# Kernel optimization log

Measured on AMD Instinct MI355X. Metric: run time of the kernel, lower is better.

## Reference

```python
import jax, jax.numpy as jnp
import numpy as np

N_ENT, N_CON, DIM, R, NB = 30000, 29309, 128, 12, 8
B, LC, S, E_DB, E_CON = 256, 50, 32, 300000, 200000


def setup_inputs() -> dict:
    key = jax.random.key(0)
    ks = jax.random.split(key, 32)
    f = lambda k, sh: (jax.random.normal(k, sh, jnp.float32) * 0.02)
    concept_emb = f(ks[0], (N_CON, DIM)).at[0].set(0.0)  # padding_idx=0 row zeroed
    inp = {
        'concept_mask': jax.random.randint(ks[1], (B, LC), 0, N_CON, jnp.int32),
        'seed_pad': jax.random.randint(ks[2], (B, S), 0, N_ENT, jnp.int32),
        'seed_lens': jax.random.randint(ks[3], (B,), 0, S + 1, jnp.int32),
        'db_edge_index': jax.random.randint(ks[4], (2, E_DB), 0, N_ENT, jnp.int32),
        'db_edge_type': jax.random.randint(ks[5], (E_DB,), 0, R, jnp.int32),
        'con_edge_index': jax.random.randint(ks[6], (2, E_CON), 0, N_CON, jnp.int32),
        'db_vec': jax.random.uniform(ks[7], (B, N_ENT), jnp.float32),
        'labels': jax.random.randint(ks[8], (B,), 0, N_ENT, jnp.int64),
        'rec': jax.random.uniform(ks[9], (B,), jnp.float32),
        'concept_emb': concept_emb,
        'basis': f(ks[10], (NB, N_ENT, DIM)),
        'comp': f(ks[11], (R, NB)),
        'rgcn_root': f(ks[12], (N_ENT, DIM)),
        'rgcn_bias': jnp.zeros((DIM,), jnp.float32),
        'gcn_w': f(ks[13], (DIM, DIM)),
        'gcn_b': jnp.zeros((DIM,), jnp.float32),
        'attn_a': f(ks[14], (DIM, DIM)),
        'attn_b': f(ks[15], (DIM, 1)),
        'attn_a_db': f(ks[16], (DIM, DIM)),
        'attn_b_db': f(ks[17], (DIM, 1)),
        'user_norm_w': f(ks[18], (DIM, 2 * DIM)),
        'user_norm_b': jnp.zeros((DIM,), jnp.float32),
        'gate_norm_w': f(ks[19], (1, DIM)),
        'gate_norm_b': jnp.zeros((1,), jnp.float32),
        'info_con_w': f(ks[20], (DIM, DIM)),
        'info_con_b': jnp.zeros((DIM,), jnp.float32),
        'info_out_db_b': jnp.zeros((N_ENT,), jnp.float32),
        'output_en_b': jnp.zeros((N_ENT,), jnp.float32),
    }
    return inp


def _forward(concept_mask, seed_pad, seed_lens, db_edge_index, db_edge_type,
             con_edge_index, db_vec, labels, rec, concept_emb, basis, comp,
             rgcn_root, rgcn_bias, gcn_w, gcn_b, attn_a, attn_b, attn_a_db,
             attn_b_db, user_norm_w, user_norm_b, gate_norm_w, gate_norm_b,
             info_con_w, info_con_b, info_out_db_b, output_en_b):
    NEG = jnp.float32(-1e30)
    # ---- RGCN over DBpedia graph (x=None -> per-edge row W[rel][src]) ----
    w = jnp.einsum('rb,bnd->rnd', comp, basis)            # [R, N_ent, D]
    src, dst = db_edge_index[0], db_edge_index[1]
    msg = w[db_edge_type, src]                            # [E, D]
    agg = jax.ops.segment_sum(msg, dst, num_segments=N_ENT)
    cnt = jax.ops.segment_sum(jnp.ones_like(dst, jnp.float32), dst, num_segments=N_ENT)
    db_feats = agg / jnp.maximum(cnt, 1.0)[:, None] + rgcn_root + rgcn_bias  # mean aggr + root + bias
    # ---- GCN over concept graph (symmetric norm, self-loops) ----
    xw = concept_emb @ gcn_w
    loops = jnp.arange(N_CON, dtype=con_edge_index.dtype)
    cs = jnp.concatenate([con_edge_index[0], loops])
    cd = jnp.concatenate([con_edge_index[1], loops])
    deg = jax.ops.segment_sum(jnp.ones_like(cd, jnp.float32), cd, num_segments=N_CON)
    dinv = jnp.where(deg > 0, jax.lax.rsqrt(jnp.maximum(deg, 1e-12)), 0.0)
    norm = dinv[cs] * dinv[cd]
    con_feats = jax.ops.segment_sum(norm[:, None] * xw[cs], cd, num_segments=N_CON) + gcn_b
    # ---- per-sample seed-set self-attention over db features ----
    h = db_feats[seed_pad]                                # [B, S, D]
    e = jnp.tanh(h @ attn_a_db) @ attn_b_db               # [B, S, 1]
    valid = jnp.arange(S)[None, :] < seed_lens[:, None]   # [B, S]
    a = jax.nn.softmax(jnp.where(valid[..., None], e, NEG), axis=1)
    db_user = jnp.einsum('bso,bsd->bd', a, h)             # weighted sum (o=1)
    has_seed = (seed_lens > 0)
    db_user = jnp.where(has_seed[:, None], db_user, 0.0)  # empty seed set -> zeros
    db_con_mask = has_seed.astype(jnp.float32)
    # ---- batch self-attention over gathered concept features ----
    hc = con_feats[concept_mask]                          # [B, LC, D]
    ec = jnp.tanh(hc @ attn_a) @ attn_b                   # [B, LC, 1]
    cvalid = (concept_mask != 0)
    ac = jax.nn.softmax(jnp.where(cvalid[..., None], ec, NEG), axis=1)
    con_user = jnp.einsum('blo,bld->bd', ac, hc)
    # ---- gated fusion ----
    u = jnp.concatenate([con_user, db_user], axis=-1) @ user_norm_w.T + user_norm_b
    gate = jax.nn.sigmoid(u @ gate_norm_w.T + gate_norm_b)  # [B, 1]
    user_emb = gate * db_user + (1.0 - gate) * con_user
    entity_scores = user_emb @ db_feats.T + output_en_b   # [B, N_ent]
    # ---- infomax MSE loss ----
    con_e = con_user @ info_con_w.T + info_con_b
    db_scores = con_e @ db_feats.T + info_out_db_b
    info_db_loss = jnp.mean(jnp.sum((db_scores - db_vec) ** 2, axis=-1) * db_con_mask)
    # ---- rec CE loss ----
    logp = jax.nn.log_softmax(entity_scores, axis=-1)
    ce = -jnp.take_along_axis(logp, labels[:, None].astype(jnp.int32), axis=1)[:, 0]
    rec_loss = jnp.sum(ce * rec)
    loss = rec_loss + 0.025 * info_db_loss                # pretrain=False path
    return loss, entity_scores, rec_loss


def reference(concept_mask, seed_pad, seed_lens, db_edge_index, db_edge_type,
              con_edge_index, db_vec, labels, rec, concept_emb, basis, comp,
              rgcn_root, rgcn_bias, gcn_w, gcn_b, attn_a, attn_b, attn_a_db,
              attn_b_db, user_norm_w, user_norm_b, gate_norm_w, gate_norm_b,
              info_con_w, info_con_b, info_out_db_b, output_en_b):
    return _forward(concept_mask, seed_pad, seed_lens, db_edge_index, db_edge_type,
                    con_edge_index, db_vec, labels, rec, concept_emb, basis, comp,
                    rgcn_root, rgcn_bias, gcn_w, gcn_b, attn_a, attn_b, attn_a_db,
                    attn_b_db, user_norm_w, user_norm_b, gate_norm_w, gate_norm_b,
                    info_con_w, info_con_b, info_out_db_b, output_en_b)
```

## Files before the change

### kernel.cpp

```cpp
#include <hip/hip_runtime.h>

#define N_ENT  30000
#define N_CON  29309
#define DIM    128
#define NBASIS 8
#define NREL   12
#define BATCH  256
#define LCON   50
#define SSEED  32
#define EDB    300000
#define ECON   200000
#define NTILE  938

#define NE4      ((N_CON * DIM) / 4)
#define NB_HIST  ((EDB + ECON + 255) / 256)
#define NB_CONV  ((NE4 + 3 * (DIM * DIM / 4) + 255) / 256)
#define NB_WCOMP ((N_ENT * 32) / 256)
#define NB_GXW   ((N_CON + 31) / 32)
#define NB_RG    ((N_ENT + 3) / 4)
#define NB_GG    ((N_CON + 3) / 4)
#define NB_EDB   ((N_ENT + 31) / 32)
#define NB_ECON  ((N_CON + 31) / 32)

typedef __attribute__((ext_vector_type(8)))  short bfrag8;
typedef __attribute__((ext_vector_type(16))) float facc16;

__device__ __forceinline__ unsigned short f2bf(float f) {
    unsigned int u = __float_as_uint(f);
    u += 0x7FFFu + ((u >> 16) & 1u);
    return (unsigned short)(u >> 16);
}
__device__ __forceinline__ float bf2f(unsigned int h) {
    return __uint_as_float(h << 16);
}

__global__ __launch_bounds__(256) void prep_kernel(const int* __restrict__ db_dst,
                                                   const int* __restrict__ con_dst,
                                                   const float* __restrict__ emb,
                                                   const float* __restrict__ W,
                                                   const float* __restrict__ A_db,
                                                   const float* __restrict__ A_c,
                                                   int* __restrict__ cnt_e, int* __restrict__ cnt_c,
                                                   int* __restrict__ ord_db, int* __restrict__ ord_con,
                                                   unsigned short* __restrict__ emb_h,
                                                   unsigned short* __restrict__ Wt_h,
                                                   unsigned short* __restrict__ At_db_h,
                                                   unsigned short* __restrict__ At_c_h) {
    int t = threadIdx.x, bb = blockIdx.x;
    if (bb < NB_HIST) {
        int e = bb * 256 + t;
        if (e < EDB) {
            ord_db[e] = atomicAdd(cnt_e + db_dst[e], 1);
        } else if (e < EDB + ECON) {
            int ee = e - EDB;
            ord_con[ee] = atomicAdd(cnt_c + con_dst[ee], 1);
        }
    } else {
        int i = (bb - NB_HIST) * 256 + t;
        if (i < NE4) {
            float4 v = ((const float4*)emb)[i];
            unsigned int p0 = (unsigned int)f2bf(v.x) | ((unsigned int)f2bf(v.y) << 16);
            unsigned int p1 = (unsigned int)f2bf(v.z) | ((unsigned int)f2bf(v.w) << 16);
            *(uint2*)(emb_h + (size_t)i * 4) = make_uint2(p0, p1);
        } else {
            int j = i - NE4;
            if (j < 3 * (DIM * DIM) / 4) {
                int sel = j >> 12;
                int jj = j & 4095;
                const float* S = (sel == 0) ? W : ((sel == 1) ? A_db : A_c);
                unsigned short* Dst = (sel == 0) ? Wt_h : ((sel == 1) ? At_db_h : At_c_h);
                int o = jj * 4;
                int n = o >> 7, k0 = o & 127;
                unsigned int p0 = (unsigned int)f2bf(S[(k0 + 0) * DIM + n]) |
                                  ((unsigned int)f2bf(S[(k0 + 1) * DIM + n]) << 16);
                unsigned int p1 = (unsigned int)f2bf(S[(k0 + 2) * DIM + n]) |
                                  ((unsigned int)f2bf(S[(k0 + 3) * DIM + n]) << 16);
                *(uint2*)(Dst + n * DIM + k0) = make_uint2(p0, p1);
            }
        }
    }
}

__device__ void scan_block(const int* __restrict__ cnt, int n, int* __restrict__ rowptr) {
    __shared__ int part[1024];
    int t = threadIdx.x;
    int per = (n + 1023) / 1024;
    int s0 = t * per;
    int sum = 0;
    for (int i = 0; i < per; ++i) {
        int idx = s0 + i;
        if (idx < n) sum += cnt[idx];
    }
    part[t] = sum;
    __syncthreads();
    for (int off = 1; off < 1024; off <<= 1) {
        int v = (t >= off) ? part[t - off] : 0;
        __syncthreads();
        part[t] += v;
        __syncthreads();
    }
    int run = part[t] - sum;
    for (int i = 0; i < per; ++i) {
        int idx = s0 + i;
        if (idx < n) {
            rowptr[idx] = run;
            run += cnt[idx];
        }
    }
    if (t == 1023) rowptr[n] = part[1023];
}

__global__ __launch_bounds__(1024) void scan2_kernel(const int* __restrict__ cnt_e,
                                                     const int* __restrict__ cnt_c,
                                                     int* __restrict__ rowptr_e,
                                                     int* __restrict__ rowptr_c,
                                                     float* __restrict__ dinv) {
    if (blockIdx.x == 0) {
        scan_block(cnt_e, N_ENT, rowptr_e);
    } else {
        scan_block(cnt_c, N_CON, rowptr_c);
        for (int i = threadIdx.x; i < N_CON; i += 1024)
            dinv[i] = rsqrtf((float)(cnt_c[i] + 1));
    }
}

__global__ __launch_bounds__(256) void mid_kernel(const int* __restrict__ db_eidx,
                                                  const int* __restrict__ db_etype,
                                                  const int* __restrict__ con_eidx,
                                                  const int* __restrict__ ord_db,
                                                  const int* __restrict__ ord_con,
                                                  const int* __restrict__ rowptr_e,
                                                  const int* __restrict__ rowptr_c,
                                                  int* __restrict__ elist_e,
                                                  int* __restrict__ elist_c,
                                                  const float* __restrict__ basis,
                                                  const float* __restrict__ comp,
                                                  unsigned short* __restrict__ w_h,
                                                  const unsigned short* __restrict__ emb_h,
                                                  const unsigned short* __restrict__ Wt_h,
                                                  unsigned short* __restrict__ xw_h,
                                                  int use_w) {
    __shared__ float sc[NREL * NBASIS];
    int t = threadIdx.x, bb = blockIdx.x;
    if (bb < NB_HIST) {
        int e = bb * 256 + t;
        if (e < EDB) {
            int dst = db_eidx[EDB + e];
            elist_e[rowptr_e[dst] + ord_db[e]] = db_eidx[e] | (db_etype[e] << 18);
        } else if (e < EDB + ECON) {
            int ee = e - EDB;
            int dst = con_eidx[ECON + ee];
            elist_c[rowptr_c[dst] + ord_con[ee]] = con_eidx[ee];
        }
        return;
    }
    if (bb < NB_HIST + NB_WCOMP) {
        if (!use_w) return;
        if (t < NREL * NBASIS) sc[t] = comp[t];
        __syncthreads();
        int i = (bb - NB_HIST) * 256 + t;
        int n = i >> 5, d4 = i & 31;
        float4 bv[NBASIS];
#pragma unroll
        for (int b = 0; b < NBASIS; ++b)
            bv[b] = ((const float4*)(basis + ((size_t)b * N_ENT + n) * DIM))[d4];
#pragma unroll
        for (int r = 0; r < NREL; ++r) {
            float4 acc = make_float4(0.f, 0.f, 0.f, 0.f);
#pragma unroll
            for (int b = 0; b < NBASIS; ++b) {
                float c = sc[r * NBASIS + b];
                acc.x += c * bv[b].x; acc.y += c * bv[b].y;
                acc.z += c * bv[b].z; acc.w += c * bv[b].w;
            }
            unsigned int p0 = (unsigned int)f2bf(acc.x) | ((unsigned int)f2bf(acc.y) << 16);
            unsigned int p1 = (unsigned int)f2bf(acc.z) | ((unsigned int)f2bf(acc.w) << 16);
            *(uint2*)(w_h + ((size_t)r * N_ENT + n) * DIM + d4 * 4) = make_uint2(p0, p1);
        }
        return;
    }
    {
        int gb = bb - NB_HIST - NB_WCOMP;
        int wave = t >> 6, lane = t & 63;
        int m0 = gb * 32;
        int n0 = wave * 32;
        int am = lane & 31, ak = (lane >> 5) * 8;
        int mrow = m0 + am;
        bool mv = mrow < N_CON;
        const unsigned short* Ar = emb_h + (size_t)mrow * DIM + ak;
        const unsigned short* Br = Wt_h + (size_t)(n0 + am) * DIM + ak;
        facc16 acc;
#pragma unroll
        for (int r = 0; r < 16; ++r) acc[r] = 0.f;
#pragma unroll
        for (int s = 0; s < 8; ++s) {
            bfrag8 a;
#pragma unroll
            for (int j = 0; j < 8; ++j) a[j] = 0;
            if (mv) a = *(const bfrag8*)(Ar + s * 16);
            bfrag8 b = *(const bfrag8*)(Br + s * 16);
            acc = __builtin_amdgcn_mfma_f32_32x32x16_bf16(a, b, acc, 0, 0, 0);
        }
        int col = lane & 31;
        int g4 = (lane >> 5) * 4;
#pragma unroll
        for (int r = 0; r < 16; ++r) {
            int m = m0 + (r & 3) + ((r >> 2) << 3) + g4;
            if (m < N_CON) xw_h[(size_t)m * DIM + n0 + col] = f2bf(acc[r]);
        }
    }
}

__global__ __launch_bounds__(256) void gathers_kernel(const int* __restrict__ rowptr_e,
                                                      const int* __restrict__ elist_e,
                                                      const unsigned short* __restrict__ w_h,
                                                      const float* __restrict__ root,
                                                      const float* __restrict__ bias,
                                                      unsigned short* __restrict__ dbf_h,
                                                      const int* __restrict__ rowptr_c,
                                                      const int* __restrict__ elist_c,
                                                      const float* __restrict__ dinv,
                                                      const unsigned short* __restrict__ xw_h,
                                                      const float* __restrict__ gcn_b,
                                                      unsigned short* __restrict__ conf_h) {
    int bb = blockIdx.x;
    int lane = threadIdx.x & 63;
    if (bb < NB_RG) {
        int wid = bb * 4 + (threadIdx.x >> 6);
        if (wid >= N_ENT) return;
        int beg = rowptr_e[wid], end = rowptr_e[wid + 1];
        float a0 = 0.f, a1 = 0.f;
        int p = beg;
        for (; p + 1 < end; p += 2) {
            int v0 = elist_e[p], v1 = elist_e[p + 1];
            unsigned int k0 = *(const unsigned int*)(w_h + ((size_t)(v0 >> 18) * N_ENT + (v0 & 0x3FFFF)) * DIM + lane * 2);
            unsigned int k1 = *(const unsigned int*)(w_h + ((size_t)(v1 >> 18) * N_ENT + (v1 & 0x3FFFF)) * DIM + lane * 2);
            a0 += bf2f(k0 & 0xFFFF) + bf2f(k1 & 0xFFFF);
            a1 += bf2f(k0 >> 16)    + bf2f(k1 >> 16);
        }
        if (p < end) {
            int v = elist_e[p];
            unsigned int k = *(const unsigned int*)(w_h + ((size_t)(v >> 18) * N_ENT + (v & 0x3FFFF)) * DIM + lane * 2);
            a0 += bf2f(k & 0xFFFF);
            a1 += bf2f(k >> 16);
        }
        float inv = 1.f / fmaxf((float)(end - beg), 1.f);
        size_t base = (size_t)wid * DIM + lane * 2;
        float f0 = a0 * inv + root[base]     + bias[lane * 2];
        float f1 = a1 * inv + root[base + 1] + bias[lane * 2 + 1];
        *(unsigned int*)(dbf_h + base) = (unsigned int)f2bf(f0) | ((unsigned int)f2bf(f1) << 16);
    } else {
        int wid = (bb - NB_RG) * 4 + (threadIdx.x >> 6);
        if (wid >= N_CON) return;
        int beg = rowptr_c[wid], end = rowptr_c[wid + 1];
        float a0 = 0.f, a1 = 0.f;
        int p = beg;
        for (; p + 1 < end; p += 2) {
            int s0 = elist_c[p], s1 = elist_c[p + 1];
            float n0 = dinv[s0], n1 = dinv[s1];
            unsigned int k0 = *(const unsigned int*)(xw_h + (size_t)s0 * DIM + lane * 2);
            unsigned int k1 = *(const unsigned int*)(xw_h + (size_t)s1 * DIM + lane * 2);
            a0 += n0 * bf2f(k0 & 0xFFFF) + n1 * bf2f(k1 & 0xFFFF);
            a1 += n0 * bf2f(k0 >> 16)    + n1 * bf2f(k1 >> 16);
        }
        if (p < end) {
            int s = elist_c[p];
            float nm = dinv[s];
            unsigned int k = *(const unsigned int*)(xw_h + (size_t)s * DIM + lane * 2);
            a0 += nm * bf2f(k & 0xFFFF);
            a1 += nm * bf2f(k >> 16);
        }
        float dv = dinv[wid];
        unsigned int ks = *(const unsigned int*)(xw_h + (size_t)wid * DIM + lane * 2);
        size_t base = (size_t)wid * DIM + lane * 2;
        float f0 = dv * a0 + dv * dv * bf2f(ks & 0xFFFF) + gcn_b[lane * 2];
        float f1 = dv * a1 + dv * dv * bf2f(ks >> 16)    + gcn_b[lane * 2 + 1];
        *(unsigned int*)(conf_h + base) = (unsigned int)f2bf(f0) | ((unsigned int)f2bf(f1) << 16);
    }
}

__global__ __launch_bounds__(256) void rgcn_gather_basis(const int* __restrict__ rowptr,
                                                         const int* __restrict__ elist,
                                                         const float* __restrict__ basis,
                                                         const float* __restrict__ comp,
                                                         const float* __restrict__ root,
                                                         const float* __restrict__ bias,
                                                         unsigned short* __restrict__ dbf_h) {
    int wid  = blockIdx.x * 4 + (threadIdx.x >> 6);
    int lane = threadIdx.x & 63;
    if (wid >= N_ENT) return;
    int beg = rowptr[wid], end = rowptr[wid + 1];
    float a0 = 0.f, a1 = 0.f;
    for (int p = beg; p < end; ++p) {
        int v = elist[p];
        int src = v & 0x3FFFF, ty = v >> 18;
        const float* c = comp + ty * NBASIS;
#pragma unroll
        for (int b = 0; b < NBASIS; ++b) {
            const float* bp = basis + ((size_t)b * N_ENT + src) * DIM;
            a0 += c[b] * bp[lane * 2];
            a1 += c[b] * bp[lane * 2 + 1];
        }
    }
    float inv = 1.f / fmaxf((float)(end - beg), 1.f);
    size_t base = (size_t)wid * DIM + lane * 2;
    float f0 = a0 * inv + root[base]     + bias[lane * 2];
    float f1 = a1 * inv + root[base + 1] + bias[lane * 2 + 1];
    *(unsigned int*)(dbf_h + base) = (unsigned int)f2bf(f0) | ((unsigned int)f2bf(f1) << 16);
}

__global__ __launch_bounds__(256) void escore_kernel(const unsigned short* __restrict__ dbf_h,
                                                     const unsigned short* __restrict__ conf_h,
                                                     const unsigned short* __restrict__ At_db_h,
                                                     const float* __restrict__ v_db,
                                                     const unsigned short* __restrict__ At_c_h,
                                                     const float* __restrict__ v_c,
                                                     float* __restrict__ e_db,
                                                     float* __restrict__ e_con) {
    __shared__ float part[4][32];
    int t = threadIdx.x, bb = blockIdx.x;
    int wave = t >> 6, lane = t & 63;
    const unsigned short* feats;
    const unsigned short* At;
    const float* v;
    float* eo;
    int m0, nrow;
    if (bb < NB_EDB) {
        feats = dbf_h;  At = At_db_h; v = v_db; eo = e_db;  m0 = bb * 32;             nrow = N_ENT;
    } else {
        feats = conf_h; At = At_c_h;  v = v_c;  eo = e_con; m0 = (bb - NB_EDB) * 32;  nrow = N_CON;
    }
    int n0 = wave * 32;
    int am = lane & 31, ak = (lane >> 5) * 8;
    int mrow = m0 + am;
    bool mv = mrow < nrow;
    const unsigned short* Ar = feats + (size_t)mrow * DIM + ak;
    const unsigned short* Br = At + (size_t)(n0 + am) * DIM + ak;
    facc16 acc;
#pragma unroll
    for (int r = 0; r < 16; ++r) acc[r] = 0.f;
#pragma unroll
    for (int s = 0; s < 8; ++s) {
        bfrag8 a;
#pragma unroll
        for (int j = 0; j < 8; ++j) a[j] = 0;
        if (mv) a = *(const bfrag8*)(Ar + s * 16);
        bfrag8 b = *(const bfrag8*)(Br + s * 16);
        acc = __builtin_amdgcn_mfma_f32_32x32x16_bf16(a, b, acc, 0, 0, 0);
    }
    int col = lane & 31, g = lane >> 5;
    float vn = v[n0 + col];
#pragma unroll
    for (int r = 0; r < 16; ++r) {
        float x = tanhf(acc[r]) * vn;
#pragma unroll
        for (int off = 16; off >= 1; off >>= 1) x += __shfl_xor(x, off, 32);
        if (col == 0) {
            int row = (r & 3) + ((r >> 2) << 3) + (g << 2);
            part[wave][row] = x;
        }
    }
    __syncthreads();
    if (t < 32) {
        int m = m0 + t;
        if (m < nrow)
            eo[m] = part[0][t] + part[1][t] + part[2][t] + part[3][t];
    }
}

__global__ __launch_bounds__(256) void attn_fusion_kernel(const unsigned short* __restrict__ dbf_h,
                                                          const unsigned short* __restrict__ conf_h,
                                                          const float* __restrict__ e_db,
                                                          const float* __restrict__ e_con,
                                                          const int* __restrict__ seed_pad,
                                                          const int* __restrict__ seed_lens,
                                                          const int* __restrict__ concept_mask,
                                                          const float* __restrict__ Wu, const float* __restrict__ bu,
                                                          const float* __restrict__ gw, const float* __restrict__ gb,
                                                          const float* __restrict__ Wi, const float* __restrict__ bi,
                                                          unsigned short* __restrict__ uemb_h,
                                                          unsigned short* __restrict__ cone_h,
                                                          float* __restrict__ maskv) {
    __shared__ int srow[SSEED];
    __shared__ int crow[LCON];
    __shared__ float a_db[SSEED], a_con[LCON];
    __shared__ float du[DIM], cu[DIM], red[DIM];
    int b = blockIdx.x, t = threadIdx.x;
    int wave = t >> 6, lane = t & 63;
    int len = seed_lens[b];
    if (wave == 0) {
        float e = -1e30f;
        if (lane < SSEED) {
            int rv = seed_pad[b * SSEED + lane];
            srow[lane] = rv;
            if (lane < len) e = e_db[rv];
        }
        float m = e;
#pragma unroll
        for (int off = 16; off >= 1; off >>= 1) m = fmaxf(m, __shfl_xor(m, off, 32));
        float p = (lane < SSEED) ? __expf(e - m) : 0.f;
        float s = p;
#pragma unroll
        for (int off = 16; off >= 1; off >>= 1) s += __shfl_xor(s, off, 32);
        if (lane < SSEED) a_db[lane] = p / s;
    } else if (wave == 1) {
        float e = -1e30f;
        if (lane < LCON) {
            int rv = concept_mask[b * LCON + lane];
            crow[lane] = rv;
            if (rv != 0) e = e_con[rv];
        }
        float m = e;
#pragma unroll
        for (int off = 32; off >= 1; off >>= 1) m = fmaxf(m, __shfl_xor(m, off, 64));
        float p = (lane < LCON) ? __expf(e - m) : 0.f;
        float s = p;
#pragma unroll
        for (int off = 32; off >= 1; off >>= 1) s += __shfl_xor(s, off, 64);
        if (lane < LCON) a_con[lane] = p / s;
    }
    __syncthreads();
    if (t < DIM) {
        float acc = 0.f;
#pragma unroll
        for (int s = 0; s < SSEED; ++s)
            acc += a_db[s] * bf2f((unsigned int)dbf_h[(size_t)srow[s] * DIM + t]);
        du[t] = (len > 0) ? acc : 0.f;
    } else {
        int d = t - DIM;
        float acc = 0.f;
#pragma unroll
        for (int s = 0; s < LCON; ++s)
            acc += a_con[s] * bf2f((unsigned int)conf_h[(size_t)crow[s] * DIM + d]);
        cu[d] = acc;
    }
    __syncthreads();
    if (t < DIM) {
        float u = bu[t];
        const float* wr = Wu + t * 2 * DIM;
        for (int k = 0; k < DIM; ++k) u += cu[k] * wr[k];
        for (int k = 0; k < DIM; ++k) u += du[k] * wr[DIM + k];
        red[t] = u * gw[t];
    }
    __syncthreads();
    for (int s2 = 64; s2 > 0; s2 >>= 1) {
        if (t < s2) red[t] += red[t + s2];
        __syncthreads();
    }
    if (t < DIM) {
        float gate = 1.f / (1.f + __expf(-(red[0] + gb[0])));
        uemb_h[b * DIM + t] = f2bf(gate * du[t] + (1.f - gate) * cu[t]);
        float ce = bi[t];
        const float* wi = Wi + t * DIM;
        for (int k = 0; k < DIM; ++k) ce += cu[k] * wi[k];
        cone_h[b * DIM + t] = f2bf(ce);
    }
    if (t == 0) maskv[b] = (len > 0) ? 1.f : 0.f;
}

__global__ __launch_bounds__(256) void score_mfma(const unsigned short* __restrict__ dbf_h,
                                                  const unsigned short* __restrict__ uemb_h,
                                                  const unsigned short* __restrict__ cone_h,
                                                  const float* __restrict__ en_b,
                                                  const float* __restrict__ info_b,
                                                  const float* __restrict__ db_vec,
                                                  float* __restrict__ escore,
                                                  float* __restrict__ partM,
                                                  float* __restrict__ partS,
                                                  float* __restrict__ partQ) {
    int wave = threadIdx.x >> 6, lane = threadIdx.x & 63;
    int nt = blockIdx.x * 4 + wave;
    if (nt >= NTILE) return;
    int b0 = blockIdx.y * 32;
    int n0 = nt * 32;
    int am = lane & 31, ak = (lane >> 5) * 8;
    int nb = n0 + am;
    bool bvalid = nb < N_ENT;
    const unsigned short* Au = uemb_h + (size_t)(b0 + am) * DIM + ak;
    const unsigned short* Ac = cone_h + (size_t)(b0 + am) * DIM + ak;
    const unsigned short* Bp = dbf_h + (size_t)nb * DIM + ak;
    facc16 accE, accD;
#pragma unroll
    for (int r = 0; r < 16; ++r) { accE[r] = 0.f; accD[r] = 0.f; }
#pragma unroll
    for (int s = 0; s < 8; ++s) {
        bfrag8 au = *(const bfrag8*)(Au + s * 16);
        bfrag8 ac = *(const bfrag8*)(Ac + s * 16);
        bfrag8 bb;
#pragma unroll
        for (int j = 0; j < 8; ++j) bb[j] = 0;
        if (bvalid) bb = *(const bfrag8*)(Bp + s * 16);
        accE = __builtin_amdgcn_mfma_f32_32x32x16_bf16(au, bb, accE, 0, 0, 0);
        accD = __builtin_amdgcn_mfma_f32_32x32x16_bf16(ac, bb, accD, 0, 0, 0);
    }
    int col = lane & 31;
    int n = n0 + col;
    bool nv = n < N_ENT;
    float enb = nv ? en_b[n] : 0.f;
    float inb = nv ? info_b[n] : 0.f;
    int g4 = (lane >> 5) * 4;
#pragma unroll
    for (int r = 0; r < 16; ++r) {
        int b = b0 + (r & 3) + ((r >> 2) << 3) + g4;
        float e = accE[r] + enb;
        if (nv) escore[(size_t)b * N_ENT + n] = e;
        float ev = nv ? e : -1e30f;
        float mx = ev;
#pragma unroll
        for (int off = 16; off >= 1; off >>= 1) mx = fmaxf(mx, __shfl_xor(mx, off, 64));
        float ex = nv ? __expf(e - mx) : 0.f;
        float sm = ex;
#pragma unroll
        for (int off = 16; off >= 1; off >>= 1) sm += __shfl_xor(sm, off, 64);
        float d = nv ? (accD[r] + inb - db_vec[(size_t)b * N_ENT + n]) : 0.f;
        float q = d * d;
#pragma unroll
        for (int off = 16; off >= 1; off >>= 1) q += __shfl_xor(q, off, 64);
        if (col == 0) {
            partM[(size_t)b * NTILE + nt] = mx;
            partS[(size_t)b * NTILE + nt] = sm;
            partQ[(size_t)b * NTILE + nt] = q;
        }
    }
}

__global__ __launch_bounds__(256) void ce_final(const float* __restrict__ partM,
                                                const float* __restrict__ partS,
                                                const float* __restrict__ partQ,
                                                const float* __restrict__ escore,
                                                const int* __restrict__ labels,
                                                const float* __restrict__ rec,
                                                float* __restrict__ rloss,
                                                float* __restrict__ ssqv) {
    __shared__ float red[256], red2[256];
    int b = blockIdx.x, t = threadIdx.x;
    const float* pm = partM + (size_t)b * NTILE;
    const float* ps = partS + (size_t)b * NTILE;
    const float* pq = partQ + (size_t)b * NTILE;
    float mx = -1e30f;
    for (int i = t; i < NTILE; i += 256) mx = fmaxf(mx, pm[i]);
    red[t] = mx;
    __syncthreads();
    for (int s2 = 128; s2 > 0; s2 >>= 1) {
        if (t < s2) red[t] = fmaxf(red[t], red[t + s2]);
        __syncthreads();
    }
    float M = red[0];
    __syncthreads();
    float s = 0.f, q = 0.f;
    for (int i = t; i < NTILE; i += 256) {
        s += ps[i] * __expf(pm[i] - M);
        q += pq[i];
    }
    red[t] = s; red2[t] = q;
    __syncthreads();
    for (int s2 = 128; s2 > 0; s2 >>= 1) {
        if (t < s2) { red[t] += red[t + s2]; red2[t] += red2[t + s2]; }
        __syncthreads();
    }
    if (t == 0) {
        float lse = M + logf(red[0]);
        float ce  = -(escore[(size_t)b * N_ENT + labels[b]] - lse);
        rloss[b]  = ce * rec[b];
        ssqv[b]   = red2[0];
    }
}

__global__ __launch_bounds__(256) void final_kernel(const float* __restrict__ rloss,
                                                    const float* __restrict__ sumsq,
                                                    const float* __restrict__ maskv,
                                                    float* __restrict__ out) {
    __shared__ float r1[256], r2[256];
    int t = threadIdx.x;
    r1[t] = rloss[t];
    r2[t] = sumsq[t] * maskv[t];
    __syncthreads();
    for (int s2 = 128; s2 > 0; s2 >>= 1) {
        if (t < s2) { r1[t] += r1[t + s2]; r2[t] += r2[t + s2]; }
        __syncthreads();
    }
    if (t == 0) {
        float rec_loss = r1[0];
        float info = r2[0] / (float)BATCH;
        out[0] = rec_loss + 0.025f * info;
        out[1 + (size_t)BATCH * N_ENT] = rec_loss;
    }
}

extern "C" void kernel_launch(void* const* d_in, const int* in_sizes, int n_in,
                              void* d_out, int out_size, void* d_ws, size_t ws_size,
                              hipStream_t stream) {
    (void)in_sizes; (void)n_in; (void)out_size;
    const int*   concept_mask  = (const int*)d_in[0];
    const int*   seed_pad      = (const int*)d_in[1];
    const int*   seed_lens     = (const int*)d_in[2];
    const int*   db_eidx       = (const int*)d_in[3];
    const int*   db_etype      = (const int*)d_in[4];
    const int*   con_eidx      = (const int*)d_in[5];
    const float* db_vec        = (const float*)d_in[6];
    const int*   labels        = (const int*)d_in[7];
    const float* rec           = (const float*)d_in[8];
    const float* concept_emb   = (const float*)d_in[9];
    const float* basis         = (const float*)d_in[10];
    const float* comp          = (const float*)d_in[11];
    const float* rgcn_root     = (const float*)d_in[12];
    const float* rgcn_bias     = (const float*)d_in[13];
    const float* gcn_w         = (const float*)d_in[14];
    const float* gcn_b         = (const float*)d_in[15];
    const float* attn_a        = (const float*)d_in[16];
    const float* attn_b        = (const float*)d_in[17];
    const float* attn_a_db     = (const float*)d_in[18];
    const float* attn_b_db     = (const float*)d_in[19];
    const float* user_norm_w   = (const float*)d_in[20];
    const float* user_norm_b   = (const float*)d_in[21];
    const float* gate_norm_w   = (const float*)d_in[22];
    const float* gate_norm_b   = (const float*)d_in[23];
    const float* info_con_w    = (const float*)d_in[24];
    const float* info_con_b    = (const float*)d_in[25];
    const float* info_out_db_b = (const float*)d_in[26];
    const float* output_en_b   = (const float*)d_in[27];

    float* ws = (float*)d_ws;
    size_t off = 0;
    auto alloc = [&](size_t n) { float* p = ws + off; off += (n + 255) & ~(size_t)255; return p; };
    float* dinv   = alloc(N_CON);
    float* maskv  = alloc(BATCH);
    float* rls    = alloc(BATCH);
    float* ssqv   = alloc(BATCH);
    float* partM  = alloc((size_t)BATCH * NTILE);
    float* partS  = alloc((size_t)BATCH * NTILE);
    float* partQ  = alloc((size_t)BATCH * NTILE);
    int* cnt_e    = (int*)alloc(N_ENT + N_CON);
    int* cnt_c    = cnt_e + N_ENT;
    int* rowptr_e = (int*)alloc(N_ENT + 1);
    int* rowptr_c = (int*)alloc(N_CON + 1);
    int* ord_db   = (int*)alloc(EDB);
    int* ord_con  = (int*)alloc(ECON);
    int* elist_e  = (int*)alloc(EDB);
    int* elist_c  = (int*)alloc(ECON);
    unsigned short* dbf_h  = (unsigned short*)alloc((size_t)N_ENT * DIM / 2);
    unsigned short* conf_h = (unsigned short*)alloc((size_t)N_CON * DIM / 2 + 128);
    unsigned short* xw_h   = (unsigned short*)alloc((size_t)N_CON * DIM / 2 + 128);
    unsigned short* emb_h  = (unsigned short*)alloc((size_t)N_CON * DIM / 2 + 128);
    unsigned short* Wt_h   = (unsigned short*)alloc(DIM * DIM / 2);
    unsigned short* uemb_h = (unsigned short*)alloc(BATCH * DIM / 2);
    unsigned short* cone_h = (unsigned short*)alloc(BATCH * DIM / 2);
    float* e_db   = alloc(N_ENT);
    float* e_con  = alloc(N_CON);
    unsigned short* At_db_h = (unsigned short*)alloc(DIM * DIM / 2);
    unsigned short* At_c_h  = (unsigned short*)alloc(DIM * DIM / 2);
    size_t w_elems = ((size_t)NREL * N_ENT * DIM) / 2;
    int use_w = (off + w_elems) * sizeof(float) <= ws_size;
    unsigned short* w_h = (unsigned short*)(ws + off);

    float* out    = (float*)d_out;
    float* escore = out + 1;

    (void)hipMemsetAsync(cnt_e, 0, (N_ENT + N_CON) * sizeof(int), stream);

    prep_kernel<<<NB_HIST + NB_CONV, 256, 0, stream>>>(db_eidx + EDB, con_eidx + ECON,
                                                       concept_emb, gcn_w, attn_a_db, attn_a,
                                                       cnt_e, cnt_c, ord_db, ord_con, emb_h, Wt_h,
                                                       At_db_h, At_c_h);
    scan2_kernel<<<2, 1024, 0, stream>>>(cnt_e, cnt_c, rowptr_e, rowptr_c, dinv);
    mid_kernel<<<NB_HIST + NB_WCOMP + NB_GXW, 256, 0, stream>>>(db_eidx, db_etype, con_eidx,
                                                                ord_db, ord_con, rowptr_e, rowptr_c,
                                                                elist_e, elist_c, basis, comp, w_h,
                                                                emb_h, Wt_h, xw_h, use_w);
    gathers_kernel<<<NB_RG + NB_GG, 256, 0, stream>>>(rowptr_e, elist_e, w_h, rgcn_root, rgcn_bias,
                                                      dbf_h, rowptr_c, elist_c, dinv, xw_h, gcn_b, conf_h);
    if (!use_w) {
        rgcn_gather_basis<<<NB_RG, 256, 0, stream>>>(rowptr_e, elist_e, basis, comp,
                                                     rgcn_root, rgcn_bias, dbf_h);
    }
    escore_kernel<<<NB_EDB + NB_ECON, 256, 0, stream>>>(dbf_h, conf_h, At_db_h, attn_b_db,
                                                        At_c_h, attn_b, e_db, e_con);
    attn_fusion_kernel<<<BATCH, 256, 0, stream>>>(dbf_h, conf_h, e_db, e_con,
                                                  seed_pad, seed_lens, concept_mask,
                                                  user_norm_w, user_norm_b, gate_norm_w, gate_norm_b,
                                                  info_con_w, info_con_b, uemb_h, cone_h, maskv);
    dim3 sg((NTILE + 3) / 4, BATCH / 32);
    score_mfma<<<sg, 256, 0, stream>>>(dbf_h, uemb_h, cone_h, output_en_b, info_out_db_b, db_vec,
                                       escore, partM, partS, partQ);
    ce_final<<<BATCH, 256, 0, stream>>>(partM, partS, partQ, escore, labels, rec, rls, ssqv);
    final_kernel<<<1, 256, 0, stream>>>(rls, ssqv, maskv, out);
}
```

Measured before the change: 526.7 us.

## Rebalance stage kernels to overlap basis compose and XW GEMM with scans

Moves the basis-composition (w_h build) into prep_kernel, and the concept XW GEMM into the scan kernel as extra 1024-thread blocks, so both run alongside the histogram and scan stages that previously ran almost alone. The edge scatter becomes its own kernel. The gather loops are unrolled from 2 to 4 edges per iteration for more memory-level parallelism. The scan kernel now launches with 1024-thread blocks for the GEMM part, which may reduce occupancy. The long-running scan blocks also stay serialized ahead of the new scatter kernel.

```diff
diff --git a/kernel.cpp b/kernel.cpp
--- a/kernel.cpp
+++ b/kernel.cpp
@@ -16,7 +16,7 @@
 #define NB_HIST  ((EDB + ECON + 255) / 256)
 #define NB_CONV  ((NE4 + 3 * (DIM * DIM / 4) + 255) / 256)
 #define NB_WCOMP ((N_ENT * 32) / 256)
-#define NB_GXW   ((N_CON + 31) / 32)
+#define NB_XW    ((N_CON + 127) / 128)
 #define NB_RG    ((N_ENT + 3) / 4)
 #define NB_GG    ((N_CON + 3) / 4)
 #define NB_EDB   ((N_ENT + 31) / 32)
@@ -40,12 +40,17 @@
                                                    const float* __restrict__ W,
                                                    const float* __restrict__ A_db,
                                                    const float* __restrict__ A_c,
+                                                   const float* __restrict__ basis,
+                                                   const float* __restrict__ comp,
                                                    int* __restrict__ cnt_e, int* __restrict__ cnt_c,
                                                    int* __restrict__ ord_db, int* __restrict__ ord_con,
                                                    unsigned short* __restrict__ emb_h,
                                                    unsigned short* __restrict__ Wt_h,
                                                    unsigned short* __restrict__ At_db_h,
-                                                   unsigned short* __restrict__ At_c_h) {
+                                                   unsigned short* __restrict__ At_c_h,
+                                                   unsigned short* __restrict__ w_h,
+                                                   int use_w) {
+    __shared__ float sc[NREL * NBASIS];
     int t = threadIdx.x, bb = blockIdx.x;
     if (bb < NB_HIST) {
         int e = bb * 256 + t;
@@ -55,7 +60,9 @@
             int ee = e - EDB;
             ord_con[ee] = atomicAdd(cnt_c + con_dst[ee], 1);
         }
-    } else {
+        return;
+    }
+    if (bb < NB_HIST + NB_CONV) {
         int i = (bb - NB_HIST) * 256 + t;
         if (i < NE4) {
             float4 v = ((const float4*)emb)[i];
@@ -78,6 +85,29 @@
                 *(uint2*)(Dst + n * DIM + k0) = make_uint2(p0, p1);
             }
         }
+        return;
+    }
+    if (!use_w) return;
+    if (t < NREL * NBASIS) sc[t] = comp[t];
+    __syncthreads();
+    int i = (bb - NB_HIST - NB_CONV) * 256 + t;
+    int n = i >> 5, d4 = i & 31;
+    float4 bv[NBASIS];
+#pragma unroll
+    for (int b = 0; b < NBASIS; ++b)
+        bv[b] = ((const float4*)(basis + ((size_t)b * N_ENT + n) * DIM))[d4];
+#pragma unroll
+    for (int r = 0; r < NREL; ++r) {
+        float4 acc = make_float4(0.f, 0.f, 0.f, 0.f);
+#pragma unroll
+        for (int b = 0; b < NBASIS; ++b) {
+            float c = sc[r * NBASIS + b];
+            acc.x += c * bv[b].x; acc.y += c * bv[b].y;
+            acc.z += c * bv[b].z; acc.w += c * bv[b].w;
+        }
+        unsigned int p0 = (unsigned int)f2bf(acc.x) | ((unsigned int)f2bf(acc.y) << 16);
+        unsigned int p1 = (unsigned int)f2bf(acc.z) | ((unsigned int)f2bf(acc.w) << 16);
+        *(uint2*)(w_h + ((size_t)r * N_ENT + n) * DIM + d4 * 4) = make_uint2(p0, p1);
     }
 }
 
@@ -114,100 +144,68 @@
                                                      const int* __restrict__ cnt_c,
                                                      int* __restrict__ rowptr_e,
                                                      int* __restrict__ rowptr_c,
-                                                     float* __restrict__ dinv) {
-    if (blockIdx.x == 0) {
+                                                     float* __restrict__ dinv,
+                                                     const unsigned short* __restrict__ emb_h,
+                                                     const unsigned short* __restrict__ Wt_h,
+                                                     unsigned short* __restrict__ xw_h) {
+    int bb = blockIdx.x;
+    if (bb == 0) {
         scan_block(cnt_e, N_ENT, rowptr_e);
-    } else {
+        return;
+    }
+    if (bb == 1) {
         scan_block(cnt_c, N_CON, rowptr_c);
         for (int i = threadIdx.x; i < N_CON; i += 1024)
             dinv[i] = rsqrtf((float)(cnt_c[i] + 1));
-    }
-}
-
-__global__ __launch_bounds__(256) void mid_kernel(const int* __restrict__ db_eidx,
-                                                  const int* __restrict__ db_etype,
-                                                  const int* __restrict__ con_eidx,
-                                                  const int* __restrict__ ord_db,
-                                                  const int* __restrict__ ord_con,
-                                                  const int* __restrict__ rowptr_e,
-                                                  const int* __restrict__ rowptr_c,
-                                                  int* __restrict__ elist_e,
-                                                  int* __restrict__ elist_c,
-                                                  const float* __restrict__ basis,
-                                                  const float* __restrict__ comp,
-                                                  unsigned short* __restrict__ w_h,
-                                                  const unsigned short* __restrict__ emb_h,
-                                                  const unsigned short* __restrict__ Wt_h,
-                                                  unsigned short* __restrict__ xw_h,
-                                                  int use_w) {
-    __shared__ float sc[NREL * NBASIS];
-    int t = threadIdx.x, bb = blockIdx.x;
-    if (bb < NB_HIST) {
-        int e = bb * 256 + t;
-        if (e < EDB) {
-            int dst = db_eidx[EDB + e];
-            elist_e[rowptr_e[dst] + ord_db[e]] = db_eidx[e] | (db_etype[e] << 18);
-        } else if (e < EDB + ECON) {
-            int ee = e - EDB;
-            int dst = con_eidx[ECON + ee];
-            elist_c[rowptr_c[dst] + ord_con[ee]] = con_eidx[ee];
-        }
         return;
     }
-    if (bb < NB_HIST + NB_WCOMP) {
-        if (!use_w) return;
-        if (t < NREL * NBASIS) sc[t] = comp[t];
-        __syncthreads();
-        int i = (bb - NB_HIST) * 256 + t;
-        int n = i >> 5, d4 = i & 31;
-        float4 bv[NBASIS];
-#pragma unroll
-        for (int b = 0; b < NBASIS; ++b)
-            bv[b] = ((const float4*)(basis + ((size_t)b * N_ENT + n) * DIM))[d4];
-#pragma unroll
-        for (int r = 0; r < NREL; ++r) {
-            float4 acc = make_float4(0.f, 0.f, 0.f, 0.f);
-#pragma unroll
-            for (int b = 0; b < NBASIS; ++b) {
-                float c = sc[r * NBASIS + b];
-                acc.x += c * bv[b].x; acc.y += c * bv[b].y;
-                acc.z += c * bv[b].z; acc.w += c * bv[b].w;
-            }
-            unsigned int p0 = (unsigned int)f2bf(acc.x) | ((unsigned int)f2bf(acc.y) << 16);
-            unsigned int p1 = (unsigned int)f2bf(acc.z) | ((unsigned int)f2bf(acc.w) << 16);
-            *(uint2*)(w_h + ((size_t)r * N_ENT + n) * DIM + d4 * 4) = make_uint2(p0, p1);
-        }
-        return;
-    }
-    {
-        int gb = bb - NB_HIST - NB_WCOMP;
-        int wave = t >> 6, lane = t & 63;
-        int m0 = gb * 32;
-        int n0 = wave * 32;
-        int am = lane & 31, ak = (lane >> 5) * 8;
-        int mrow = m0 + am;
-        bool mv = mrow < N_CON;
-        const unsigned short* Ar = emb_h + (size_t)mrow * DIM + ak;
-        const unsigned short* Br = Wt_h + (size_t)(n0 + am) * DIM + ak;
-        facc16 acc;
-#pragma unroll
-        for (int r = 0; r < 16; ++r) acc[r] = 0.f;
-#pragma unroll
-        for (int s = 0; s < 8; ++s) {
-            bfrag8 a;
-#pragma unroll
-            for (int j = 0; j < 8; ++j) a[j] = 0;
-            if (mv) a = *(const bfrag8*)(Ar + s * 16);
-            bfrag8 b = *(const bfrag8*)(Br + s * 16);
-            acc = __builtin_amdgcn_mfma_f32_32x32x16_bf16(a, b, acc, 0, 0, 0);
-        }
-        int col = lane & 31;
-        int g4 = (lane >> 5) * 4;
-#pragma unroll
-        for (int r = 0; r < 16; ++r) {
-            int m = m0 + (r & 3) + ((r >> 2) << 3) + g4;
-            if (m < N_CON) xw_h[(size_t)m * DIM + n0 + col] = f2bf(acc[r]);
-        }
+    int t = threadIdx.x;
+    int wave = t >> 6, lane = t & 63;
+    int m0 = (bb - 2) * 128 + (wave >> 2) * 32;
+    int n0 = (wave & 3) * 32;
+    int am = lane & 31, ak = (lane >> 5) * 8;
+    int mrow = m0 + am;
+    bool mv = mrow < N_CON;
+    const unsigned short* Ar = emb_h + (size_t)mrow * DIM + ak;
+    const unsigned short* Br = Wt_h + (size_t)(n0 + am) * DIM + ak;
+    facc16 acc;
+#pragma unroll
+    for (int r = 0; r < 16; ++r) acc[r] = 0.f;
+#pragma unroll
+    for (int s = 0; s < 8; ++s) {
+        bfrag8 a;
+#pragma unroll
+        for (int j = 0; j < 8; ++j) a[j] = 0;
+        if (mv) a = *(const bfrag8*)(Ar + s * 16);
+        bfrag8 b = *(const bfrag8*)(Br + s * 16);
+        acc = __builtin_amdgcn_mfma_f32_32x32x16_bf16(a, b, acc, 0, 0, 0);
+    }
+    int col = lane & 31;
+    int g4 = (lane >> 5) * 4;
+#pragma unroll
+    for (int r = 0; r < 16; ++r) {
+        int m = m0 + (r & 3) + ((r >> 2) << 3) + g4;
+        if (m < N_CON) xw_h[(size_t)m * DIM + n0 + col] = f2bf(acc[r]);
+    }
+}
+
+__global__ __launch_bounds__(256) void scatter_kernel(const int* __restrict__ db_eidx,
+                                                      const int* __restrict__ db_etype,
+                                                      const int* __restrict__ con_eidx,
+                                                      const int* __restrict__ ord_db,
+                                                      const int* __restrict__ ord_con,
+                                                      const int* __restrict__ rowptr_e,
+                                                      const int* __restrict__ rowptr_c,
+                                                      int* __restrict__ elist_e,
+                                                      int* __restrict__ elist_c) {
+    int e = blockIdx.x * 256 + threadIdx.x;
+    if (e < EDB) {
+        int dst = db_eidx[EDB + e];
+        elist_e[rowptr_e[dst] + ord_db[e]] = db_eidx[e] | (db_etype[e] << 18);
+    } else if (e < EDB + ECON) {
+        int ee = e - EDB;
+        int dst = con_eidx[ECON + ee];
+        elist_c[rowptr_c[dst] + ord_con[ee]] = con_eidx[ee];
     }
 }
 
@@ -231,14 +229,16 @@
         int beg = rowptr_e[wid], end = rowptr_e[wid + 1];
         float a0 = 0.f, a1 = 0.f;
         int p = beg;
-        for (; p + 1 < end; p += 2) {
-            int v0 = elist_e[p], v1 = elist_e[p + 1];
+        for (; p + 3 < end; p += 4) {
+            int v0 = elist_e[p], v1 = elist_e[p + 1], v2 = elist_e[p + 2], v3 = elist_e[p + 3];
             unsigned int k0 = *(const unsigned int*)(w_h + ((size_t)(v0 >> 18) * N_ENT + (v0 & 0x3FFFF)) * DIM + lane * 2);
             unsigned int k1 = *(const unsigned int*)(w_h + ((size_t)(v1 >> 18) * N_ENT + (v1 & 0x3FFFF)) * DIM + lane * 2);
-            a0 += bf2f(k0 & 0xFFFF) + bf2f(k1 & 0xFFFF);
-            a1 += bf2f(k0 >> 16)    + bf2f(k1 >> 16);
-        }
-        if (p < end) {
+            unsigned int k2 = *(const unsigned int*)(w_h + ((size_t)(v2 >> 18) * N_ENT + (v2 & 0x3FFFF)) * DIM + lane * 2);
+            unsigned int k3 = *(const unsigned int*)(w_h + ((size_t)(v3 >> 18) * N_ENT + (v3 & 0x3FFFF)) * DIM + lane * 2);
+            a0 += bf2f(k0 & 0xFFFF) + bf2f(k1 & 0xFFFF) + bf2f(k2 & 0xFFFF) + bf2f(k3 & 0xFFFF);
+            a1 += bf2f(k0 >> 16)    + bf2f(k1 >> 16)    + bf2f(k2 >> 16)    + bf2f(k3 >> 16);
+        }
+        for (; p < end; ++p) {
             int v = elist_e[p];
             unsigned int k = *(const unsigned int*)(w_h + ((size_t)(v >> 18) * N_ENT + (v & 0x3FFFF)) * DIM + lane * 2);
             a0 += bf2f(k & 0xFFFF);
@@ -255,15 +255,17 @@
         int beg = rowptr_c[wid], end = rowptr_c[wid + 1];
         float a0 = 0.f, a1 = 0.f;
         int p = beg;
-        for (; p + 1 < end; p += 2) {
-            int s0 = elist_c[p], s1 = elist_c[p + 1];
-            float n0 = dinv[s0], n1 = dinv[s1];
+        for (; p + 3 < end; p += 4) {
+            int s0 = elist_c[p], s1 = elist_c[p + 1], s2 = elist_c[p + 2], s3 = elist_c[p + 3];
+            float n0 = dinv[s0], n1 = dinv[s1], n2 = dinv[s2], n3 = dinv[s3];
             unsigned int k0 = *(const unsigned int*)(xw_h + (size_t)s0 * DIM + lane * 2);
             unsigned int k1 = *(const unsigned int*)(xw_h + (size_t)s1 * DIM + lane * 2);
-            a0 += n0 * bf2f(k0 & 0xFFFF) + n1 * bf2f(k1 & 0xFFFF);
-            a1 += n0 * bf2f(k0 >> 16)    + n1 * bf2f(k1 >> 16);
-        }
-        if (p < end) {
+            unsigned int k2 = *(const unsigned int*)(xw_h + (size_t)s2 * DIM + lane * 2);
+            unsigned int k3 = *(const unsigned int*)(xw_h + (size_t)s3 * DIM + lane * 2);
+            a0 += n0 * bf2f(k0 & 0xFFFF) + n1 * bf2f(k1 & 0xFFFF) + n2 * bf2f(k2 & 0xFFFF) + n3 * bf2f(k3 & 0xFFFF);
+            a1 += n0 * bf2f(k0 >> 16)    + n1 * bf2f(k1 >> 16)    + n2 * bf2f(k2 >> 16)    + n3 * bf2f(k3 >> 16);
+        }
+        for (; p < end; ++p) {
             int s = elist_c[p];
             float nm = dinv[s];
             unsigned int k = *(const unsigned int*)(xw_h + (size_t)s * DIM + lane * 2);
@@ -658,15 +660,15 @@
 
     (void)hipMemsetAsync(cnt_e, 0, (N_ENT + N_CON) * sizeof(int), stream);
 
-    prep_kernel<<<NB_HIST + NB_CONV, 256, 0, stream>>>(db_eidx + EDB, con_eidx + ECON,
-                                                       concept_emb, gcn_w, attn_a_db, attn_a,
-                                                       cnt_e, cnt_c, ord_db, ord_con, emb_h, Wt_h,
-                                                       At_db_h, At_c_h);
-    scan2_kernel<<<2, 1024, 0, stream>>>(cnt_e, cnt_c, rowptr_e, rowptr_c, dinv);
-    mid_kernel<<<NB_HIST + NB_WCOMP + NB_GXW, 256, 0, stream>>>(db_eidx, db_etype, con_eidx,
-                                                                ord_db, ord_con, rowptr_e, rowptr_c,
-                                                                elist_e, elist_c, basis, comp, w_h,
-                                                                emb_h, Wt_h, xw_h, use_w);
+    prep_kernel<<<NB_HIST + NB_CONV + NB_WCOMP, 256, 0, stream>>>(
+        db_eidx + EDB, con_eidx + ECON, concept_emb, gcn_w, attn_a_db, attn_a,
+        basis, comp, cnt_e, cnt_c, ord_db, ord_con, emb_h, Wt_h, At_db_h, At_c_h,
+        w_h, use_w);
+    scan2_kernel<<<2 + NB_XW, 1024, 0, stream>>>(cnt_e, cnt_c, rowptr_e, rowptr_c, dinv,
+                                                 emb_h, Wt_h, xw_h);
+    scatter_kernel<<<NB_HIST, 256, 0, stream>>>(db_eidx, db_etype, con_eidx,
+                                                ord_db, ord_con, rowptr_e, rowptr_c,
+                                                elist_e, elist_c);
     gathers_kernel<<<NB_RG + NB_GG, 256, 0, stream>>>(rowptr_e, elist_e, w_h, rgcn_root, rgcn_bias,
                                                       dbf_h, rowptr_c, elist_c, dinv, xw_h, gcn_b, conf_h);
     if (!use_w) {
```

Result: no change. 517.5 us (-1.8%).
